# Kernel tuning notes

Hardware: AMD Instinct MI355X
Metric: run time of the kernel (lower is better)

The kernel has to match this reference:

```python
import jax, jax.numpy as jnp
import numpy as np

NUM_CLASSES = 50257
TOP_K = 5
BATCH = 8192


def setup_inputs() -> dict:
    key = jax.random.key(0)
    k1, k2 = jax.random.split(key)
    teacher_logits = jax.random.normal(k1, (BATCH, NUM_CLASSES), dtype=jnp.float32)
    labels = jax.random.randint(k2, (BATCH,), 0, NUM_CLASSES, dtype=jnp.int64)
    return {"teacher_logits": teacher_logits, "labels": labels}


def reference(teacher_logits, labels):
    """Vectorized hard-negative mining: mask out each sample's true label,
    then take top-K class indices from the remaining (negative) logits.
    Returns int32 indices of shape (B, TOP_K), matching the per-sample
    List[int] output of the torch module (indices are into the full class axis)."""
    B = teacher_logits.shape[0]
    # Set the true-label logit to -inf so it can never be selected by top_k.
    masked = teacher_logits.at[jnp.arange(B), labels].set(-jnp.inf)
    _, idx = jax.lax.top_k(masked, TOP_K)  # (B, TOP_K)
    return idx
```

## Files before the change

### kernel.cpp

```cpp
#include <hip/hip_runtime.h>
#include <math.h>


constexpr int kC = 50257;

__global__ __launch_bounds__(256)
void hnm_topk_kernel(const float* __restrict__ logits,
                     const int* __restrict__ labels,
                     int* __restrict__ out,
                     int B)
{
    const int lane = threadIdx.x & 63;
    const int row  = blockIdx.x * 4 + (threadIdx.x >> 6);
    if (row >= B) return;

    const int label = labels[row];
    const float* __restrict__ rp = logits + (size_t)row * kC;

    float v0 = -INFINITY, v1 = -INFINITY, v2 = -INFINITY, v3 = -INFINITY, v4 = -INFINITY;
    int   i0 = 0, i1 = 0, i2 = 0, i3 = 0, i4 = 0;

#define TRY_INSERT(VAL, ID)                                                       \
    do {                                                                          \
        float _v = (VAL); int _id = (ID);                                         \
        if (_v > v4 && _id != label) {                                            \
            if (_v > v2) {                                                        \
                if (_v > v0)      { v4=v3;i4=i3; v3=v2;i3=i2; v2=v1;i2=i1;        \
                                    v1=v0;i1=i0; v0=_v;i0=_id; }                  \
                else if (_v > v1) { v4=v3;i4=i3; v3=v2;i3=i2; v2=v1;i2=i1;        \
                                    v1=_v;i1=_id; }                               \
                else              { v4=v3;i4=i3; v3=v2;i3=i2; v2=_v;i2=_id; }     \
            } else {                                                              \
                if (_v > v3)      { v4=v3;i4=i3; v3=_v;i3=_id; }                  \
                else              { v4=_v;i4=_id; }                               \
            }                                                                     \
        }                                                                         \
    } while (0)

    const int s = (4 - (row & 3)) & 3;
    if (lane < s) {
        TRY_INSERT(rp[lane], lane);
    }

    const int nvec = (kC - s) >> 2;
    const float4* __restrict__ vp = (const float4*)(rp + s);
    for (int j = lane; j < nvec; j += 64) {
        float4 q = vp[j];
        int base = s + (j << 2);
        TRY_INSERT(q.x, base + 0);
        TRY_INSERT(q.y, base + 1);
        TRY_INSERT(q.z, base + 2);
        TRY_INSERT(q.w, base + 3);
    }

    {
        int t = s + (nvec << 2) + lane;
        if (t < kC) TRY_INSERT(rp[t], t);
    }

#pragma unroll
    for (int k = 0; k < 5; ++k) {
        float bv = v0; int bi = i0; int bl = lane;
#pragma unroll
        for (int d = 32; d >= 1; d >>= 1) {
            float ov = __shfl_xor(bv, d, 64);
            int   oi = __shfl_xor(bi, d, 64);
            int   ol = __shfl_xor(bl, d, 64);
            if (ov > bv || (ov == bv && oi < bi)) { bv = ov; bi = oi; bl = ol; }
        }
        if (lane == 0) out[row * 5 + k] = bi;
        if (lane == bl) {
            v0=v1;i0=i1; v1=v2;i1=i2; v2=v3;i2=i3; v3=v4;i3=i4; v4=-INFINITY;
        }
    }
#undef TRY_INSERT
}

extern "C" void kernel_launch(void* const* d_in, const int* in_sizes, int n_in,
                              void* d_out, int out_size, void* d_ws, size_t ws_size,
                              hipStream_t stream)
{
    const float* logits = (const float*)d_in[0];
    const int*   labels = (const int*)d_in[1];
    int*         out    = (int*)d_out;
    const int B = in_sizes[1];

    dim3 block(256);
    dim3 grid((B + 3) / 4);
    hipLaunchKernelGGL(hnm_topk_kernel, grid, block, 0, stream,
                       logits, labels, out, B);
}
```

Before: 284.3 us.

## Keep top-6 per lane, filter label at merge, unroll loads with nontemporal hints

Removes the per-element label comparison from the hot scan by keeping six candidates per lane and dropping the label during the wave-level merge, where six rounds are run and only five non-label results are written. The main loop is also unrolled by two so each lane has two 16-byte loads in flight, and those loads use nontemporal hints to avoid polluting the cache on streamed data. The kernel is memory-bound, so the savings in compare work may not show; the larger insertion network adds registers and a sixth shuffle-reduction round.

```diff
diff --git a/kernel.cpp b/kernel.cpp
--- a/kernel.cpp
+++ b/kernel.cpp
@@ -3,6 +3,8 @@
 
 
 constexpr int kC = 50257;
+
+typedef float vf4 __attribute__((ext_vector_type(4)));
 
 __global__ __launch_bounds__(256)
 void hnm_topk_kernel(const float* __restrict__ logits,
@@ -17,49 +19,60 @@
     const int label = labels[row];
     const float* __restrict__ rp = logits + (size_t)row * kC;
 
-    float v0 = -INFINITY, v1 = -INFINITY, v2 = -INFINITY, v3 = -INFINITY, v4 = -INFINITY;
-    int   i0 = 0, i1 = 0, i2 = 0, i3 = 0, i4 = 0;
+    float v0=-INFINITY, v1=-INFINITY, v2=-INFINITY, v3=-INFINITY, v4=-INFINITY, v5=-INFINITY;
+    int   i0=0, i1=0, i2=0, i3=0, i4=0, i5=0;
 
-#define TRY_INSERT(VAL, ID)                                                       \
+#define INS(VAL, ID)                                                              \
     do {                                                                          \
-        float _v = (VAL); int _id = (ID);                                         \
-        if (_v > v4 && _id != label) {                                            \
+        float _v = (VAL);                                                         \
+        if (_v > v5) {                                                            \
+            int _id = (ID);                                                       \
             if (_v > v2) {                                                        \
-                if (_v > v0)      { v4=v3;i4=i3; v3=v2;i3=i2; v2=v1;i2=i1;        \
-                                    v1=v0;i1=i0; v0=_v;i0=_id; }                  \
-                else if (_v > v1) { v4=v3;i4=i3; v3=v2;i3=i2; v2=v1;i2=i1;        \
-                                    v1=_v;i1=_id; }                               \
-                else              { v4=v3;i4=i3; v3=v2;i3=i2; v2=_v;i2=_id; }     \
+                if (_v > v1) {                                                    \
+                    if (_v > v0) { v5=v4;i5=i4; v4=v3;i4=i3; v3=v2;i3=i2;         \
+                                   v2=v1;i2=i1; v1=v0;i1=i0; v0=_v;i0=_id; }      \
+                    else         { v5=v4;i5=i4; v4=v3;i4=i3; v3=v2;i3=i2;         \
+                                   v2=v1;i2=i1; v1=_v;i1=_id; }                   \
+                } else           { v5=v4;i5=i4; v4=v3;i4=i3; v3=v2;i3=i2;         \
+                                   v2=_v;i2=_id; }                                \
             } else {                                                              \
-                if (_v > v3)      { v4=v3;i4=i3; v3=_v;i3=_id; }                  \
-                else              { v4=_v;i4=_id; }                               \
+                if (_v > v4) {                                                    \
+                    if (_v > v3) { v5=v4;i5=i4; v4=v3;i4=i3; v3=_v;i3=_id; }      \
+                    else         { v5=v4;i5=i4; v4=_v;i4=_id; }                   \
+                } else           { v5=_v;i5=_id; }                                \
             }                                                                     \
         }                                                                         \
     } while (0)
 
     const int s = (4 - (row & 3)) & 3;
-    if (lane < s) {
-        TRY_INSERT(rp[lane], lane);
-    }
+    if (lane < s) INS(rp[lane], lane);
 
     const int nvec = (kC - s) >> 2;
-    const float4* __restrict__ vp = (const float4*)(rp + s);
-    for (int j = lane; j < nvec; j += 64) {
-        float4 q = vp[j];
-        int base = s + (j << 2);
-        TRY_INSERT(q.x, base + 0);
-        TRY_INSERT(q.y, base + 1);
-        TRY_INSERT(q.z, base + 2);
-        TRY_INSERT(q.w, base + 3);
+    const vf4* __restrict__ vp = (const vf4*)(rp + s);
+
+    int j = lane;
+    for (; j + 64 < nvec; j += 128) {
+        vf4 q0 = __builtin_nontemporal_load(vp + j);
+        vf4 q1 = __builtin_nontemporal_load(vp + j + 64);
+        int b0 = s + (j << 2);
+        INS(q0.x, b0 + 0); INS(q0.y, b0 + 1); INS(q0.z, b0 + 2); INS(q0.w, b0 + 3);
+        int b1 = b0 + 256;
+        INS(q1.x, b1 + 0); INS(q1.y, b1 + 1); INS(q1.z, b1 + 2); INS(q1.w, b1 + 3);
+    }
+    for (; j < nvec; j += 64) {
+        vf4 q = __builtin_nontemporal_load(vp + j);
+        int b = s + (j << 2);
+        INS(q.x, b + 0); INS(q.y, b + 1); INS(q.z, b + 2); INS(q.w, b + 3);
     }
 
     {
         int t = s + (nvec << 2) + lane;
-        if (t < kC) TRY_INSERT(rp[t], t);
+        if (t < kC) INS(rp[t], t);
     }
 
+    int wr = 0;
 #pragma unroll
-    for (int k = 0; k < 5; ++k) {
+    for (int k = 0; k < 6; ++k) {
         float bv = v0; int bi = i0; int bl = lane;
 #pragma unroll
         for (int d = 32; d >= 1; d >>= 1) {
@@ -68,12 +81,16 @@
             int   ol = __shfl_xor(bl, d, 64);
             if (ov > bv || (ov == bv && oi < bi)) { bv = ov; bi = oi; bl = ol; }
         }
-        if (lane == 0) out[row * 5 + k] = bi;
+        if (bi != label) {
+            if (lane == 0 && wr < 5) out[row * 5 + wr] = bi;
+            ++wr;
+        }
         if (lane == bl) {
-            v0=v1;i0=i1; v1=v2;i1=i2; v2=v3;i2=i3; v3=v4;i3=i4; v4=-INFINITY;
+            v0=v1;i0=i1; v1=v2;i1=i2; v2=v3;i2=i3; v3=v4;i3=i4; v4=v5;i4=i5;
+            v5=-INFINITY;
         }
     }
-#undef TRY_INSERT
+#undef INS
 }
 
 extern "C" void kernel_launch(void* const* d_in, const int* in_sizes, int n_in,
```

Measured after the change: 270.1 us (median of 2 runs). 1.05x faster.
